# Kernel tuning notes

Hardware: AMD Instinct MI355X
Metric: run time of the kernel (lower is better)

Reference implementation:

```python
import jax, jax.numpy as jnp
import numpy as np

B = 64          # batch_size
H = 16384       # n_hidden
BS = 32         # block size of BlockSparseLinear
NB = H // BS    # 512 blocks per dim
NNZ = int(0.1 * NB * NB)  # 26214 nonzero blocks (density 0.1)
N_IN = 1024     # n_inputs
N_OUT = 1024    # n_outputs
STEPS = 8       # n_forward_steps


def setup_inputs() -> dict:
    key = jax.random.key(0)
    k1, k2, k3, k4, k5 = jax.random.split(key, 5)
    # kaiming-ish scale for effective fan-in = H * density
    w_scale = 1.0 / np.sqrt(H * 0.1)
    inp = jax.random.normal(k1, (B, N_IN), dtype=jnp.float32)
    blocks = jax.random.normal(k2, (NNZ, BS, BS), dtype=jnp.float32) * w_scale
    bias = jax.random.normal(k3, (H,), dtype=jnp.float32) * 0.01
    block_rows = jax.random.randint(k4, (NNZ,), 0, NB, dtype=jnp.int32)
    block_cols = jax.random.randint(k5, (NNZ,), 0, NB, dtype=jnp.int32)
    return {"inp": inp, "blocks": blocks, "bias": bias,
            "block_rows": block_rows, "block_cols": block_cols}


def _block_sparse_linear(blocks, block_rows, block_cols, bias, x):
    # x: [B, H] -> y = W_sparse @ x + bias, W stored as NNZ 32x32 blocks
    xb = x.reshape(B, NB, BS)[:, block_cols]               # [B, NNZ, BS]
    contrib = jnp.einsum('nij,bnj->nbi', blocks, xb)       # [NNZ, B, BS]
    yb = jax.ops.segment_sum(contrib, block_rows, num_segments=NB)  # [NB, B, BS]
    return yb.transpose(1, 0, 2).reshape(B, H) + bias


def reference(inp, blocks, bias, block_rows, block_cols):
    # hs = zeros[B, H]; first n_inputs slots get the input (squeeze trailing 1-dim)
    hs = jnp.zeros((B, H), dtype=inp.dtype).at[:, :N_IN].set(inp)
    for step in range(STEPS):
        hs = _block_sparse_linear(blocks, block_rows, block_cols, bias, hs)
        if step != STEPS - 1:
            hs = jax.nn.sigmoid(hs)
    # output_act = sigmoid on last n_outputs entries
    return jax.nn.sigmoid(hs[:, -N_OUT:])
```

## Files before the change

### kernel.cpp

```cpp
#include <hip/hip_runtime.h>
#include <stdint.h>

#define B_     64
#define H_     16384
#define NB_    512
#define NNZ_   26214
#define N_IN_  1024
#define N_OUT_ 1024

typedef __attribute__((ext_vector_type(8))) short    bf16x8;
typedef __attribute__((ext_vector_type(4))) float    f32x4;
typedef __attribute__((ext_vector_type(4))) unsigned int u32x4;

__device__ __forceinline__ unsigned short f2bf(float f) {
    union { unsigned int i; float f; } v; v.f = f;
    unsigned int x = v.i;
    return (unsigned short)((x + 0x7fffu + ((x >> 16) & 1u)) >> 16);
}

__device__ __forceinline__ bf16x8 ldfrag(const unsigned short* p) {
    union { u32x4 u; bf16x8 b; } cv;
    cv.u = *(const u32x4*)p;
    return cv.b;
}


__global__ void zero_cnt(int* __restrict__ cnt) { cnt[threadIdx.x] = 0; }

__global__ void hist(const int* __restrict__ rows, int* __restrict__ cnt) {
    int n = blockIdx.x * 256 + threadIdx.x;
    if (n < NNZ_) atomicAdd(&cnt[rows[n]], 1);
}

__global__ void scan_k(int* __restrict__ cnt, int* __restrict__ ptr) {
    __shared__ int tmp[NB_];
    int t = threadIdx.x;
    tmp[t] = cnt[t];
    __syncthreads();
    for (int off = 1; off < NB_; off <<= 1) {
        int v = (t >= off) ? tmp[t - off] : 0;
        __syncthreads();
        tmp[t] += v;
        __syncthreads();
    }
    if (t == 0) ptr[0] = 0;
    ptr[t + 1] = tmp[t];
    cnt[t] = 0;
}

__global__ void scatter2(const int* __restrict__ rows, const int* __restrict__ cols,
                         const int* __restrict__ ptr, int* __restrict__ cnt,
                         int2* __restrict__ pair2) {
    int n = blockIdx.x * 256 + threadIdx.x;
    if (n < NNZ_) {
        int r = rows[n];
        int pos = ptr[r] + atomicAdd(&cnt[r], 1);
        pair2[pos] = make_int2(n, cols[n]);
    }
}


__global__ __launch_bounds__(256) void conv_w(const float* __restrict__ w,
                                              unsigned short* __restrict__ wb) {
    int idx = blockIdx.x * 256 + threadIdx.x;
    float4 v = ((const float4*)w)[idx];
    union { unsigned short s[4]; uint2 d; } o;
    o.s[0] = f2bf(v.x); o.s[1] = f2bf(v.y); o.s[2] = f2bf(v.z); o.s[3] = f2bf(v.w);
    ((uint2*)wb)[idx] = o.d;
}


__global__ __launch_bounds__(256) void init_x(const float* __restrict__ inp,
                                              unsigned short* __restrict__ xb) {
    int idx = blockIdx.x * 256 + threadIdx.x;
    int b = idx >> 14;
    int h = idx & (H_ - 1);
    xb[idx] = (h < N_IN_) ? f2bf(inp[b * N_IN_ + h]) : (unsigned short)0;
}

#define MFMA8(A, Bv)                                                         \
    do {                                                                     \
        _Pragma("unroll")                                                    \
        for (int mt = 0; mt < 2; ++mt)                                       \
            _Pragma("unroll")                                                \
            for (int nt = 0; nt < 4; ++nt)                                   \
                acc[mt][nt] = __builtin_amdgcn_mfma_f32_16x16x32_bf16(       \
                                  A[mt], Bv[nt], acc[mt][nt], 0, 0, 0);      \
    } while (0)

template <bool LAST>
__global__ __launch_bounds__(256) void rowstep_k(
        const unsigned short* __restrict__ x,
        unsigned short* __restrict__ xout,
        float* __restrict__ out,
        const unsigned short* __restrict__ wb,
        const float* __restrict__ bias,
        const int2* __restrict__ pair2,
        const int* __restrict__ ptr,
        int row_base, int col_limit) {
    __shared__ int2  s_pairs[4][64];
    __shared__ float s_red[4][64][33];

    const int r    = blockIdx.x + row_base;
    const int tid  = threadIdx.x;
    const int wv   = tid >> 6;
    const int lane = tid & 63;
    const int half = lane & 15;
    const int quad = lane >> 4;

    const int beg = ptr[r], cnt = ptr[r + 1] - beg;
    const int c0 = beg + (cnt * wv) / 4;
    const int m  = beg + (cnt * (wv + 1)) / 4 - c0;

    int2 pc = make_int2(0, 0);
    bool valid = (lane < m);
    if (valid) pc = pair2[c0 + lane];
    valid = valid && (pc.y < col_limit);
    unsigned long long mask = __ballot(valid);
    if (valid) {
        int pos = __popcll(mask & ((1ull << lane) - 1ull));
        s_pairs[wv][pos] = pc;
    }
    const int mv = __popcll(mask);

    f32x4 acc[2][4] = {};

    bf16x8 A0[2], B0[4], A1[2], B1[4];
    #define LDFRAGS(A, Bv, p)                                                  \
        do {                                                                   \
            const unsigned short* wp =                                         \
                wb + (size_t)(p).x * 1024 + half * 32 + quad * 8;              \
            A[0] = ldfrag(wp);                                                 \
            A[1] = ldfrag(wp + 16 * 32);                                       \
            const unsigned short* xp =                                         \
                x + (size_t)(p).y * 32 + (size_t)half * H_ + quad * 8;         \
            Bv[0] = ldfrag(xp);                                                \
            Bv[1] = ldfrag(xp + (size_t)16 * H_);                              \
            Bv[2] = ldfrag(xp + (size_t)32 * H_);                              \
            Bv[3] = ldfrag(xp + (size_t)48 * H_);                              \
        } while (0)

    if (mv > 0) { int2 p = s_pairs[wv][0]; LDFRAGS(A0, B0, p); }
    int j = 0;
    while (j + 2 <= mv) {
        { int2 p = s_pairs[wv][j + 1]; LDFRAGS(A1, B1, p); }
        MFMA8(A0, B0);
        if (j + 2 < mv) { int2 p = s_pairs[wv][j + 2]; LDFRAGS(A0, B0, p); }
        MFMA8(A1, B1);
        j += 2;
    }
    if (j < mv) MFMA8(A0, B0);

    #pragma unroll
    for (int mt = 0; mt < 2; ++mt)
        #pragma unroll
        for (int nt = 0; nt < 4; ++nt)
            #pragma unroll
            for (int q2 = 0; q2 < 4; ++q2)
                s_red[wv][nt * 16 + half][mt * 16 + quad * 4 + q2] = acc[mt][nt][q2];
    __syncthreads();

    const int b  = tid >> 2;
    const int i0 = (tid & 3) * 8;
    float v[8];
    #pragma unroll
    for (int k = 0; k < 8; ++k)
        v[k] = s_red[0][b][i0 + k] + s_red[1][b][i0 + k]
             + s_red[2][b][i0 + k] + s_red[3][b][i0 + k]
             + bias[r * 32 + i0 + k];
    if (LAST) {
        #pragma unroll
        for (int k = 0; k < 8; ++k)
            out[(size_t)b * N_OUT_ + (r - (NB_ - N_OUT_ / 32)) * 32 + i0 + k]
                = 1.0f / (1.0f + __expf(-v[k]));
    } else {
        union { unsigned short s[8]; u32x4 u; } o;
        #pragma unroll
        for (int k = 0; k < 8; ++k)
            o.s[k] = f2bf(1.0f / (1.0f + __expf(-v[k])));
        *(u32x4*)(xout + (size_t)b * H_ + r * 32 + i0) = o.u;
    }
}


extern "C" void kernel_launch(void* const* d_in, const int* in_sizes, int n_in,
                              void* d_out, int out_size, void* d_ws, size_t ws_size,
                              hipStream_t stream) {
    const float* inp    = (const float*)d_in[0];
    const float* blocks = (const float*)d_in[1];
    const float* bias   = (const float*)d_in[2];
    const int*   rows   = (const int*)d_in[3];
    const int*   cols   = (const int*)d_in[4];
    float*       out    = (float*)d_out;

    char* ws = (char*)d_ws;
    unsigned short* wbf = (unsigned short*)ws;
    unsigned short* x0  = (unsigned short*)(ws + 53686272u);
    unsigned short* x1  = (unsigned short*)(ws + 53686272u + 2097152u);
    char*  idxbase      = ws + 53686272u + 2u * 2097152u;
    int*   rowptr = (int*)(idxbase);
    int*   rowcnt = (int*)(idxbase + 4096);
    int2*  pair2  = (int2*)(idxbase + 8192);

    zero_cnt<<<1, NB_, 0, stream>>>(rowcnt);
    hist<<<(NNZ_ + 255) / 256, 256, 0, stream>>>(rows, rowcnt);
    scan_k<<<1, NB_, 0, stream>>>(rowcnt, rowptr);
    scatter2<<<(NNZ_ + 255) / 256, 256, 0, stream>>>(rows, cols, rowptr, rowcnt, pair2);

    conv_w<<<NNZ_, 256, 0, stream>>>(blocks, wbf);

    init_x<<<(B_ * H_) / 256, 256, 0, stream>>>(inp, x0);

    unsigned short* cur = x0;
    unsigned short* nxt = x1;
    rowstep_k<false><<<NB_, 256, 0, stream>>>(cur, nxt, nullptr, wbf, bias,
                                              pair2, rowptr, 0, 32);
    { unsigned short* t = cur; cur = nxt; nxt = t; }
    for (int s = 1; s < 7; ++s) {
        rowstep_k<false><<<NB_, 256, 0, stream>>>(cur, nxt, nullptr, wbf, bias,
                                                  pair2, rowptr, 0, NB_);
        unsigned short* t = cur; cur = nxt; nxt = t;
    }
    rowstep_k<true><<<N_OUT_ / 32, 256, 0, stream>>>(cur, nullptr, out, wbf, bias,
                                                     pair2, rowptr,
                                                     NB_ - N_OUT_ / 32, NB_);
}
```

Baseline: 345.8 us.

## Store activations block-major and split each row block over eight waves

```diff
diff --git a/kernel.cpp b/kernel.cpp
--- a/kernel.cpp
+++ b/kernel.cpp
@@ -73,8 +73,10 @@
 __global__ __launch_bounds__(256) void init_x(const float* __restrict__ inp,
                                               unsigned short* __restrict__ xb) {
     int idx = blockIdx.x * 256 + threadIdx.x;
-    int b = idx >> 14;
-    int h = idx & (H_ - 1);
+    int c = idx >> 11;
+    int b = (idx >> 5) & 63;
+    int j = idx & 31;
+    int h = c * 32 + j;
     xb[idx] = (h < N_IN_) ? f2bf(inp[b * N_IN_ + h]) : (unsigned short)0;
 }
 
@@ -89,7 +91,7 @@
     } while (0)
 
 template <bool LAST>
-__global__ __launch_bounds__(256) void rowstep_k(
+__global__ __launch_bounds__(512, 4) void rowstep_k(
         const unsigned short* __restrict__ x,
         unsigned short* __restrict__ xout,
         float* __restrict__ out,
@@ -98,8 +100,8 @@
         const int2* __restrict__ pair2,
         const int* __restrict__ ptr,
         int row_base, int col_limit) {
-    __shared__ int2  s_pairs[4][64];
-    __shared__ float s_red[4][64][33];
+    __shared__ int2  s_pairs[8][64];
+    __shared__ float s_red[8][64][33];
 
     const int r    = blockIdx.x + row_base;
     const int tid  = threadIdx.x;
@@ -109,8 +111,8 @@
     const int quad = lane >> 4;
 
     const int beg = ptr[r], cnt = ptr[r + 1] - beg;
-    const int c0 = beg + (cnt * wv) / 4;
-    const int m  = beg + (cnt * (wv + 1)) / 4 - c0;
+    const int c0 = beg + (cnt * wv) / 8;
+    const int m  = beg + (cnt * (wv + 1)) / 8 - c0;
 
     int2 pc = make_int2(0, 0);
     bool valid = (lane < m);
@@ -133,11 +135,11 @@
             A[0] = ldfrag(wp);                                                 \
             A[1] = ldfrag(wp + 16 * 32);                                       \
             const unsigned short* xp =                                         \
-                x + (size_t)(p).y * 32 + (size_t)half * H_ + quad * 8;         \
+                x + ((size_t)(p).y * 64 + half) * 32 + quad * 8;               \
             Bv[0] = ldfrag(xp);                                                \
-            Bv[1] = ldfrag(xp + (size_t)16 * H_);                              \
-            Bv[2] = ldfrag(xp + (size_t)32 * H_);                              \
-            Bv[3] = ldfrag(xp + (size_t)48 * H_);                              \
+            Bv[1] = ldfrag(xp + 16 * 32);                                      \
+            Bv[2] = ldfrag(xp + 32 * 32);                                      \
+            Bv[3] = ldfrag(xp + 48 * 32);                                      \
         } while (0)
 
     if (mv > 0) { int2 p = s_pairs[wv][0]; LDFRAGS(A0, B0, p); }
@@ -160,25 +162,28 @@
                 s_red[wv][nt * 16 + half][mt * 16 + quad * 4 + q2] = acc[mt][nt][q2];
     __syncthreads();
 
-    const int b  = tid >> 2;
-    const int i0 = (tid & 3) * 8;
-    float v[8];
+    const int b  = tid >> 3;
+    const int i0 = (tid & 7) * 4;
+    const float4 bv = *(const float4*)&bias[r * 32 + i0];
+    float v[4] = {bv.x, bv.y, bv.z, bv.w};
     #pragma unroll
-    for (int k = 0; k < 8; ++k)
-        v[k] = s_red[0][b][i0 + k] + s_red[1][b][i0 + k]
-             + s_red[2][b][i0 + k] + s_red[3][b][i0 + k]
-             + bias[r * 32 + i0 + k];
+    for (int w = 0; w < 8; ++w)
+        #pragma unroll
+        for (int k = 0; k < 4; ++k)
+            v[k] += s_red[w][b][i0 + k];
     if (LAST) {
+        float4 o;
+        o.x = 1.0f / (1.0f + __expf(-v[0]));
+        o.y = 1.0f / (1.0f + __expf(-v[1]));
+        o.z = 1.0f / (1.0f + __expf(-v[2]));
+        o.w = 1.0f / (1.0f + __expf(-v[3]));
+        *(float4*)&out[(size_t)b * N_OUT_ + (r - (NB_ - N_OUT_ / 32)) * 32 + i0] = o;
+    } else {
+        union { unsigned short s[4]; uint2 u; } o;
         #pragma unroll
-        for (int k = 0; k < 8; ++k)
-            out[(size_t)b * N_OUT_ + (r - (NB_ - N_OUT_ / 32)) * 32 + i0 + k]
-                = 1.0f / (1.0f + __expf(-v[k]));
-    } else {
-        union { unsigned short s[8]; u32x4 u; } o;
-        #pragma unroll
-        for (int k = 0; k < 8; ++k)
+        for (int k = 0; k < 4; ++k)
             o.s[k] = f2bf(1.0f / (1.0f + __expf(-v[k])));
-        *(u32x4*)(xout + (size_t)b * H_ + r * 32 + i0) = o.u;
+        *(uint2*)&xout[((size_t)r * 64 + b) * 32 + i0] = o.u;
     }
 }
 
@@ -213,15 +218,15 @@
 
     unsigned short* cur = x0;
     unsigned short* nxt = x1;
-    rowstep_k<false><<<NB_, 256, 0, stream>>>(cur, nxt, nullptr, wbf, bias,
+    rowstep_k<false><<<NB_, 512, 0, stream>>>(cur, nxt, nullptr, wbf, bias,
                                               pair2, rowptr, 0, 32);
     { unsigned short* t = cur; cur = nxt; nxt = t; }
     for (int s = 1; s < 7; ++s) {
-        rowstep_k<false><<<NB_, 256, 0, stream>>>(cur, nxt, nullptr, wbf, bias,
+        rowstep_k<false><<<NB_, 512, 0, stream>>>(cur, nxt, nullptr, wbf, bias,
                                                   pair2, rowptr, 0, NB_);
         unsigned short* t = cur; cur = nxt; nxt = t;
     }
-    rowstep_k<true><<<N_OUT_ / 32, 256, 0, stream>>>(cur, nullptr, out, wbf, bias,
+    rowstep_k<true><<<N_OUT_ / 32, 512, 0, stream>>>(cur, nullptr, out, wbf, bias,
                                                      pair2, rowptr,
                                                      NB_ - N_OUT_ / 32, NB_);
 }
```

Result: faster. 302.5 us (-12.5%).
